# Kernel optimization log

Hardware: AMD Instinct MI355X
Metric: run time of the kernel (lower is better)

Reference implementation:

```python
import jax, jax.numpy as jnp
import numpy as np

H, K, V, F = 8, 64, 192, 192  # heads, key_size, value_size, num_position_features


def central_mask_features(distances, feature_size, seq_length):
    # distances: [L] float; returns [L, feature_size]
    pow_rate = np.exp(np.log(seq_length + 1) / feature_size).astype('float32')
    center_widths = jnp.power(pow_rate, jnp.arange(1, feature_size + 1, dtype=jnp.float32)) - 1.0
    return (center_widths[None, :] > jnp.abs(distances)[:, None]).astype(jnp.float32)


def positional_features(distances, feature_size, seq_length, symmetric=False):
    num_components = 1 if symmetric else 2
    emb = central_mask_features(distances, feature_size // num_components, seq_length)
    if not symmetric:
        emb = jnp.concatenate([emb, jnp.sign(distances)[:, None] * emb], axis=-1)
    return emb  # [L, feature_size]


def relative_shift(x):
    # x: [B, H, T1, T2] with T2 = 2*T1 - 1 -> [B, H, T1, T1]
    b, h, t1, t2 = x.shape
    x = jnp.pad(x, ((0, 0), (0, 0), (0, 0), (1, 0)))  # [B,H,T1,T2+1]
    x = x.reshape(b, h, t2 + 1, t1)[:, :, 1:, :]      # drop first row
    x = x.reshape(b, h, t1, t2)
    return x[..., : (t2 + 1) // 2]


def setup_inputs() -> dict:
    key = jax.random.key(0)
    ks = jax.random.split(key, 9)
    B, T, C = 2, 1536, 1536
    s = 1.0 / np.sqrt(C).astype('float32')
    return {
        'inputs': jax.random.normal(ks[0], (B, T, C), jnp.float32),
        'Wq': jax.random.normal(ks[1], (C, H * K), jnp.float32) * s,
        'Wk': jax.random.normal(ks[2], (C, H * K), jnp.float32) * s,
        'Wv': jax.random.normal(ks[3], (C, H * V), jnp.float32) * s,
        'Wrk': jax.random.normal(ks[4], (F, H * K), jnp.float32) * (1.0 / np.sqrt(F).astype('float32')),
        'We': jax.random.normal(ks[5], (H * V, H * V), jnp.float32) * (1.0 / np.sqrt(H * V).astype('float32')),
        'be': jnp.zeros((H * V,), jnp.float32),
        'r_w_bias': jax.random.normal(ks[6], (1, H, 1, K), jnp.float32) * 0.1,
        'r_r_bias': jax.random.normal(ks[7], (1, H, 1, K), jnp.float32) * 0.1,
    }


def reference(inputs, Wq, Wk, Wv, Wrk, We, be, r_w_bias, r_r_bias):
    B, T, C = inputs.shape

    def heads(x, d):  # [B,T,H*d] -> [B,H,T,d]
        return x.reshape(B, T, H, d).transpose(0, 2, 1, 3)

    q = heads(inputs @ Wq, K) * (K ** -0.5)
    k = heads(inputs @ Wk, K)
    v = heads(inputs @ Wv, V)

    # content logits: (q + r_w_bias) k^T -> [B,H,T,T]
    content_logits = jnp.einsum('bhqk,bhmk->bhqm', q + r_w_bias, k)

    # relative position logits
    distances = jnp.arange(-T + 1, T, dtype=jnp.float32)  # [2T-1]
    pe = positional_features(distances, F, T, symmetric=False)  # [2T-1, F]
    r_k = (pe @ Wrk).reshape(2 * T - 1, H, K).transpose(1, 0, 2)  # [H, 2T-1, K]
    rel_logits = jnp.einsum('bhqk,hmk->bhqm', q + r_r_bias, r_k)  # [B,H,T,2T-1]
    rel_logits = relative_shift(rel_logits)  # [B,H,T,T]

    logits = content_logits + rel_logits
    attn = jax.nn.softmax(logits, axis=-1)
    out = jnp.einsum('bhqm,bhmv->bhqv', attn, v)  # [B,H,T,V]
    out = out.transpose(0, 2, 1, 3).reshape(B, T, H * V)
    return out @ We + be
```

## Files before the change

kernel.cpp:

```cpp
#include <hip/hip_runtime.h>
#include <math.h>

#define HB 8
#define KD 64
#define VD 192
#define BT 2
#define TT 1536
#define CC 1536
#define HK (HB*KD)
#define HV (HB*VD)
#define QKVP 2560
#define LOG2E 1.44269504088896340736f

typedef float f32x4 __attribute__((ext_vector_type(4)));
typedef __bf16 bf16x8 __attribute__((ext_vector_type(8)));
typedef uint uint2v __attribute__((ext_vector_type(2)));

static __device__ __forceinline__ ushort f2bf(float f) {
  union { float f; uint u; } v; v.f = f;
  uint r = (v.u + 0x7FFFu + ((v.u >> 16) & 1u)) >> 16;
  return (ushort)r;
}
static __device__ __forceinline__ float bf2f(ushort u) {
  union { uint u; float f; } v; v.u = ((uint)u) << 16; return v.f;
}

static __device__ __forceinline__ f32x4 mfma_bf(bf16x8 a, bf16x8 b, f32x4 c) {
  return __builtin_amdgcn_mfma_f32_16x16x32_bf16(a, b, c, 0, 0, 0);
}

static __device__ __forceinline__ void gload_lds16(const ushort* g, ushort* l) {
  __builtin_amdgcn_global_load_lds(
      (const __attribute__((address_space(1))) unsigned int*)g,
      (__attribute__((address_space(3))) unsigned int*)l, 16, 0, 0);
}

__device__ __forceinline__ void storeC(float* p, float v) { *p = v; }
__device__ __forceinline__ void storeC(ushort* p, float v) { *p = f2bf(v); }

__global__ __launch_bounds__(256) void cast_bf16(
    const float* __restrict__ in, ushort* __restrict__ out, int n4)
{
  for (int i = blockIdx.x*blockDim.x + threadIdx.x; i < n4; i += gridDim.x*blockDim.x) {
    float4 v = ((const float4*)in)[i];
    ushort4 o; o.x = f2bf(v.x); o.y = f2bf(v.y); o.z = f2bf(v.z); o.w = f2bf(v.w);
    ((ushort4*)out)[i] = o;
  }
}

__global__ void tcast(const float* __restrict__ in, ushort* __restrict__ out, int R, int C, float scale)
{
  __shared__ float tile[32][33];
  const int bx = blockIdx.x * 32;
  const int by = blockIdx.y * 32;
  const int tx = threadIdx.x, ty = threadIdx.y;
  #pragma unroll
  for (int i = 0; i < 4; ++i)
    tile[ty + i*8][tx] = in[(size_t)(by + ty + i*8)*C + bx + tx];
  __syncthreads();
  #pragma unroll
  for (int i = 0; i < 4; ++i)
    out[(size_t)(bx + ty + i*8)*R + by + tx] = f2bf(tile[tx][ty + i*8] * scale);
}

__global__ void vtrans(const ushort* __restrict__ in, ushort* __restrict__ out)
{
  __shared__ ushort tile[32][33];
  const int bx = blockIdx.x * 32;
  const int by = blockIdx.y * 32;
  const int tx = threadIdx.x, ty = threadIdx.y;
  #pragma unroll
  for (int i = 0; i < 4; ++i)
    tile[ty + i*8][tx] = in[(size_t)(by + ty + i*8)*QKVP + 1024 + bx + tx];
  __syncthreads();
  #pragma unroll
  for (int i = 0; i < 4; ++i)
    out[(size_t)(bx + ty + i*8)*(BT*TT) + by + tx] = tile[tx][ty + i*8];
}

template<bool WITH_BIAS, typename OutT>
__global__ __launch_bounds__(256) void gemm_bf16(
    const ushort* __restrict__ A, const ushort* __restrict__ Bt,
    const float* __restrict__ bias, OutT* __restrict__ C,
    int M, int N, int Kd)
{
  __shared__ __align__(16) ushort As[128*64];
  __shared__ __align__(16) ushort Bs[128*64];
  const int t = threadIdx.x;
  const int w = t >> 6, lane = t & 63;
  const int lrow = lane & 15, lk8 = lane >> 4;
  const int row0 = blockIdx.y * 128, col0 = blockIdx.x * 128;
  const int wr = (w >> 1) * 64, wc = (w & 1) * 64;

  f32x4 acc[4][4];
  #pragma unroll
  for (int m = 0; m < 4; ++m)
    #pragma unroll
    for (int n = 0; n < 4; ++n) acc[m][n] = (f32x4){0.f,0.f,0.f,0.f};

  for (int k0 = 0; k0 < Kd; k0 += 64) {
    __syncthreads();
    #pragma unroll
    for (int j = 0; j < 4; ++j) {
      const int c = (w*4 + j)*64 + lane;
      const int r = c >> 3, cp = c & 7;
      const int sc = cp ^ (r & 7);
      gload_lds16(A  + (size_t)(row0 + r)*Kd + k0 + sc*8, As + c*8);
      gload_lds16(Bt + (size_t)(col0 + r)*Kd + k0 + sc*8, Bs + c*8);
    }
    __syncthreads();
    bf16x8 af[4][2], bfv[4][2];
    #pragma unroll
    for (int m = 0; m < 4; ++m) {
      const int r = wr + m*16 + lrow;
      #pragma unroll
      for (int kh = 0; kh < 2; ++kh) {
        const int k8 = lk8 + kh*4;
        af[m][kh] = *(const bf16x8*)&As[r*64 + ((k8 ^ (r & 7)) << 3)];
      }
    }
    #pragma unroll
    for (int n = 0; n < 4; ++n) {
      const int r = wc + n*16 + lrow;
      #pragma unroll
      for (int kh = 0; kh < 2; ++kh) {
        const int k8 = lk8 + kh*4;
        bfv[n][kh] = *(const bf16x8*)&Bs[r*64 + ((k8 ^ (r & 7)) << 3)];
      }
    }
    #pragma unroll
    for (int m = 0; m < 4; ++m)
      #pragma unroll
      for (int n = 0; n < 4; ++n) {
        acc[m][n] = mfma_bf(af[m][0], bfv[n][0], acc[m][n]);
        acc[m][n] = mfma_bf(af[m][1], bfv[n][1], acc[m][n]);
      }
  }
  #pragma unroll
  for (int m = 0; m < 4; ++m)
    #pragma unroll
    for (int n = 0; n < 4; ++n) {
      const int cg = col0 + wc + n*16 + lrow;
      const float bb = WITH_BIAS ? bias[cg] : 0.f;
      #pragma unroll
      for (int r = 0; r < 4; ++r) {
        const int rg = row0 + wr + m*16 + lk8*4 + r;
        storeC(&C[(size_t)rg*N + cg], acc[m][n][r] + bb);
      }
    }
}

__global__ __launch_bounds__(256) void wrk_suffix(
    const float* __restrict__ Wrk, float* __restrict__ S1, float* __restrict__ S2)
{
  const int c = blockIdx.x*blockDim.x + threadIdx.x;
  float a1 = 0.f, a2 = 0.f;
  S1[96*HK + c] = 0.f; S2[96*HK + c] = 0.f;
  for (int i = 95; i >= 0; --i) {
    a1 += Wrk[i*HK + c];
    a2 += Wrk[(96 + i)*HK + c];
    S1[i*HK + c] = a1; S2[i*HK + c] = a2;
  }
}

__global__ __launch_bounds__(256) void relk_fill(
    const float* __restrict__ S1, const float* __restrict__ S2,
    const float* __restrict__ rrb, ushort* __restrict__ rk, float* __restrict__ c2g)
{
  __shared__ float cw[96];
  __shared__ float red[512];
  __shared__ int i0s;
  const int t = threadIdx.x;
  const int m = blockIdx.x;
  if (t < 96) {
    double pr = exp(log((double)(TT + 1)) / 96.0);
    float prf = (float)pr;
    cw[t] = (float)pow((double)prf, (double)(t + 1)) - 1.0f;
  }
  __syncthreads();
  const int d = m - (TT - 1);
  const float ad = fabsf((float)d);
  if (t == 0) {
    int i0 = 96;
    for (int i = 0; i < 96; ++i) if (cw[i] > ad) { i0 = i; break; }
    i0s = i0;
  }
  __syncthreads();
  const float sg = (d > 0) ? 1.f : (d < 0 ? -1.f : 0.f);
  const int i0 = i0s;
  for (int c = t; c < HK; c += 256) {
    const float val = S1[i0*HK + c] + sg * S2[i0*HK + c];
    const ushort vb = f2bf(val);
    rk[(size_t)m * HK + c] = vb;
    red[c] = bf2f(vb) * rrb[c];
  }
  __syncthreads();
  if (t < 8) {
    float s = 0.f;
    #pragma unroll 16
    for (int i = 0; i < 64; ++i) s += red[t*64 + i];
    c2g[(size_t)t*(2*TT - 1) + m] = s * LOG2E;
  }
}

__global__ __launch_bounds__(256) void c1_kernel(
    const ushort* __restrict__ qkv, const float* __restrict__ rwb, float* __restrict__ c1g)
{
  const int idx = blockIdx.x*256 + threadIdx.x;
  const int h = idx & 7, row = idx >> 3;
  const ushort* kr = &qkv[(size_t)row*QKVP + 512 + h*KD];
  float s = 0.f;
  #pragma unroll 16
  for (int c = 0; c < 64; ++c) s += bf2f(kr[c]) * rwb[h*KD + c];
  c1g[h*(BT*TT) + row] = s * LOG2E;
}

__global__ __launch_bounds__(256) void attn_mfma(
    const ushort* __restrict__ qkv, const ushort* __restrict__ vTg,
    const ushort* __restrict__ rk,
    const float* __restrict__ c1g, const float* __restrict__ c2g,
    ushort* __restrict__ aout)
{
  __shared__ __align__(16) ushort ktL[32*64];
  __shared__ __align__(16) ushort rkbL[64*64];
  __shared__ __align__(16) ushort vTl[192*64];
  __shared__ __align__(16) ushort Pl[32][40];
  __shared__ __align__(16) float S1[32][34];
  __shared__ __align__(16) float S2[32][66];
  __shared__ float corrl[32], linv[32];

  const int t = threadIdx.x;
  const int wv = t >> 6, lane = t & 63;
  const int lrow = lane & 15, lk8 = lane >> 4;
  const int bid = blockIdx.x;
  const int qt = bid % (TT/32);
  const int h  = (bid / (TT/32)) % HB;
  const int b  = bid / ((TT/32) * HB);
  const int q0 = qt * 32;

  bf16x8 af[2][2];
  #pragma unroll
  for (int rt = 0; rt < 2; ++rt)
    #pragma unroll
    for (int kh = 0; kh < 2; ++kh)
      af[rt][kh] = *(const bf16x8*)&qkv[((size_t)(b*TT) + q0 + rt*16 + lrow)*QKVP + h*KD + kh*32 + lk8*8];

  if (t < 32) ((uint*)rkbL)[63*32 + t] = 0;

  const int kc_r = t >> 3, kc_p = t & 7;
  const ushort* ksrc = qkv + (size_t)(b*TT + kc_r)*QKVP + 512 + h*KD + (kc_p ^ (kc_r & 7))*8;
  ushort* kdst = ktL + t*8;
  const int rr0 = t >> 3, rp0 = t & 7;
  const int rr1 = (256 + t) >> 3, rp1 = t & 7;
  const ushort* rsrc0 = rk + (size_t)(TT - 32 - q0 + rr0)*HK + h*KD + (rp0 ^ (rr0 & 7))*8;
  const ushort* rsrc1 = rk + (size_t)(TT - 32 - q0 + rr1)*HK + h*KD + (rp1 ^ (rr1 & 7))*8;
  ushort* rdst0 = rkbL + t*8;
  ushort* rdst1 = rkbL + (256 + t)*8;
  const bool rval = t < 248;
  const ushort* vsrc[6]; ushort* vdst[6];
  #pragma unroll
  for (int W = 0; W < 6; ++W) {
    const int c = W*256 + t;
    const int vd = c >> 3, cpk = c & 7;
    vsrc[W] = vTg + (size_t)(h*VD + vd)*(BT*TT) + b*TT + (cpk ^ (vd & 7))*8;
    vdst[W] = vTl + c*8;
  }

  const int jk  = (wv & 1)*16 + lrow;
  const int j2a = (wv & 1)*32 + lrow;
  const int j2b = j2a + 16;
  const int rt_ = wv >> 1;

  f32x4 acc[2][3];
  #pragma unroll
  for (int i = 0; i < 2; ++i)
    #pragma unroll
    for (int j = 0; j < 3; ++j) acc[i][j] = (f32x4){0.f, 0.f, 0.f, 0.f};
  float m_i = -1e30f, l_i = 0.f;
  const int r_s = t >> 3;
  const int vsl = t & 7;

  gload_lds16(ksrc, kdst);               ksrc += 32*QKVP;
  gload_lds16(rsrc0, rdst0);             rsrc0 += 32*HK;
  if (rval) gload_lds16(rsrc1, rdst1);
  rsrc1 += 32*HK;

  for (int it = 0; it < 48; ++it) {
    const int kt0 = it << 5;
    const int mbase = kt0 - q0 + (TT - 32);
    const float c1v  = c1g[h*(BT*TT) + b*TT + kt0 + jk];
    const float c2v0 = c2g[(size_t)h*(2*TT - 1) + mbase + j2a];
    const float c2r  = c2g[(size_t)h*(2*TT - 1) + mbase + (j2b < 63 ? j2b : 62)];
    const float c2v1 = (j2b < 63) ? c2r : 0.f;

    if ((it & 1) == 0) {
      asm volatile("s_waitcnt lgkmcnt(0)" ::: "memory");
      __builtin_amdgcn_s_barrier();
      #pragma unroll
      for (int W = 0; W < 6; ++W) { gload_lds16(vsrc[W], vdst[W]); vsrc[W] += 64; }
      asm volatile("s_waitcnt vmcnt(6)" ::: "memory");
      __builtin_amdgcn_s_barrier();
    } else {
      asm volatile("s_waitcnt vmcnt(3)" ::: "memory");
      __builtin_amdgcn_s_barrier();
    }

    {
      bf16x8 b0 = *(const bf16x8*)&ktL[jk*64 + ((lk8 ^ (jk & 7)) << 3)];
      bf16x8 b1 = *(const bf16x8*)&ktL[jk*64 + (((lk8 + 4) ^ (jk & 7)) << 3)];
      f32x4 c0 = (f32x4){0.f, 0.f, 0.f, 0.f};
      c0 = mfma_bf(af[rt_][0], b0, c0);
      c0 = mfma_bf(af[rt_][1], b1, c0);
      #pragma unroll
      for (int r = 0; r < 4; ++r) S1[rt_*16 + lk8*4 + r][jk] = c0[r] + c1v;

      bf16x8 d0 = *(const bf16x8*)&rkbL[j2a*64 + ((lk8 ^ (j2a & 7)) << 3)];
      bf16x8 d1 = *(const bf16x8*)&rkbL[j2a*64 + (((lk8 + 4) ^ (j2a & 7)) << 3)];
      f32x4 ca = (f32x4){0.f, 0.f, 0.f, 0.f};
      ca = mfma_bf(af[rt_][0], d0, ca);
      ca = mfma_bf(af[rt_][1], d1, ca);
      #pragma unroll
      for (int r = 0; r < 4; ++r) S2[rt_*16 + lk8*4 + r][j2a] = ca[r] + c2v0;

      bf16x8 e0 = *(const bf16x8*)&rkbL[j2b*64 + ((lk8 ^ (j2b & 7)) << 3)];
      bf16x8 e1 = *(const bf16x8*)&rkbL[j2b*64 + (((lk8 + 4) ^ (j2b & 7)) << 3)];
      f32x4 cb = (f32x4){0.f, 0.f, 0.f, 0.f};
      cb = mfma_bf(af[rt_][0], e0, cb);
      cb = mfma_bf(af[rt_][1], e1, cb);
      #pragma unroll
      for (int r = 0; r < 4; ++r) S2[rt_*16 + lk8*4 + r][j2b] = cb[r] + c2v1;
    }
    asm volatile("s_waitcnt lgkmcnt(0)" ::: "memory");
    __builtin_amdgcn_s_barrier();
    if (it < 47) {
      gload_lds16(ksrc, kdst);               ksrc += 32*QKVP;
      gload_lds16(rsrc0, rdst0);             rsrc0 += 32*HK;
      if (rval) gload_lds16(rsrc1, rdst1);
      rsrc1 += 32*HK;
    }
    {
      float sv[4];
      #pragma unroll
      for (int i = 0; i < 4; ++i) {
        const int j = vsl*4 + i;
        sv[i] = S1[r_s][j] + S2[r_s][j - r_s + 31];
      }
      float lmax = fmaxf(fmaxf(sv[0], sv[1]), fmaxf(sv[2], sv[3]));
      #pragma unroll
      for (int s = 1; s < 8; s <<= 1) lmax = fmaxf(lmax, __shfl_xor(lmax, s, 64));
      const bool defer = (lmax <= m_i + 8.0f);
      const float m_new = defer ? m_i : fmaxf(m_i, lmax);
      const float corr  = defer ? 1.0f : exp2f(m_i - m_new);
      const float p0 = exp2f(sv[0] - m_new), p1 = exp2f(sv[1] - m_new);
      const float p2 = exp2f(sv[2] - m_new), p3 = exp2f(sv[3] - m_new);
      uint2v pw;
      pw.x = (uint)f2bf(p0) | ((uint)f2bf(p1) << 16);
      pw.y = (uint)f2bf(p2) | ((uint)f2bf(p3) << 16);
      *(uint2v*)&Pl[r_s][vsl*4] = pw;
      float lsum = (p0 + p1) + (p2 + p3);
      #pragma unroll
      for (int s = 1; s < 8; s <<= 1) lsum += __shfl_xor(lsum, s, 64);
      l_i = l_i * corr + lsum;
      m_i = m_new;
      if (vsl == 0) corrl[r_s] = corr;
    }
    if ((it & 1) == 0) { asm volatile("s_waitcnt vmcnt(3)" ::: "memory"); }
    asm volatile("s_waitcnt lgkmcnt(0)" ::: "memory");
    __builtin_amdgcn_s_barrier();
    {
      const int kh4 = (it & 1) * 4;
      float cr[2][4];
      #pragma unroll
      for (int rt = 0; rt < 2; ++rt)
        #pragma unroll
        for (int r = 0; r < 4; ++r) cr[rt][r] = corrl[rt*16 + lk8*4 + r];
      bool need = false;
      #pragma unroll
      for (int rt = 0; rt < 2; ++rt)
        #pragma unroll
        for (int r = 0; r < 4; ++r) need |= (cr[rt][r] != 1.0f);
      if (__any(need ? 1 : 0)) {
        #pragma unroll
        for (int rt = 0; rt < 2; ++rt)
          #pragma unroll
          for (int cc = 0; cc < 3; ++cc)
            #pragma unroll
            for (int r = 0; r < 4; ++r) acc[rt][cc][r] *= cr[rt][r];
      }
      #pragma unroll
      for (int rt = 0; rt < 2; ++rt) {
        const bf16x8 pa = *(const bf16x8*)&Pl[rt*16 + lrow][lk8*8];
        #pragma unroll
        for (int cc = 0; cc < 3; ++cc) {
          const int rv = (3*wv + cc)*16 + lrow;
          const bf16x8 bv = *(const bf16x8*)&vTl[rv*64 + (((kh4 + lk8) ^ (rv & 7)) << 3)];
          acc[rt][cc] = mfma_bf(pa, bv, acc[rt][cc]);
        }
      }
    }
  }
  if (vsl == 0) linv[r_s] = 1.0f / l_i;
  __syncthreads();
  #pragma unroll
  for (int rt = 0; rt < 2; ++rt) {
    #pragma unroll
    for (int cc = 0; cc < 3; ++cc) {
      const int colg = (3*wv + cc)*16 + lrow;
      #pragma unroll
      for (int r = 0; r < 4; ++r) {
        const int rowg = rt*16 + lk8*4 + r;
        aout[((size_t)(b*TT) + q0 + rowg) * HV + h*VD + colg] = f2bf(acc[rt][cc][r] * linv[rowg]);
      }
    }
  }
}

extern "C" void kernel_launch(void* const* d_in, const int* in_sizes, int n_in,
                              void* d_out, int out_size, void* d_ws, size_t ws_size,
                              hipStream_t stream)
{
  const float* X   = (const float*)d_in[0];
  const float* Wq  = (const float*)d_in[1];
  const float* Wk  = (const float*)d_in[2];
  const float* Wv  = (const float*)d_in[3];
  const float* Wrk = (const float*)d_in[4];
  const float* We  = (const float*)d_in[5];
  const float* be  = (const float*)d_in[6];
  const float* rwb = (const float*)d_in[7];
  const float* rrb = (const float*)d_in[8];
  float* out = (float*)d_out;

  char* ws = (char*)d_ws;
  ushort* Xb    = (ushort*)ws;                       ws += (size_t)3072*1536*2;
  ushort* Wqkvt = (ushort*)ws;                       ws += (size_t)2560*1536*2;
  ushort* Wet   = (ushort*)ws;                       ws += (size_t)1536*1536*2;
  float*  S1b   = (float*)ws;                        ws += (size_t)97*512*4;
  float*  S2b   = (float*)ws;                        ws += (size_t)97*512*4;
  ushort* qkvb  = (ushort*)ws;                       ws += (size_t)3072*2560*2;
  ushort* vTgb  = (ushort*)ws;                       ws += (size_t)1536*3072*2;
  ushort* rkb   = (ushort*)ws;                       ws += (size_t)3071*512*2;
  float*  c1g   = (float*)ws;                        ws += (size_t)8*3072*4;
  float*  c2g   = (float*)ws;                        ws += (size_t)8*3071*4;
  ushort* ao    = (ushort*)ws;

  dim3 blk(256);
  cast_bf16<<<2048, blk, 0, stream>>>(X, Xb, (3072*1536)/4);
  tcast<<<dim3(512/32, 1536/32),  dim3(32,8), 0, stream>>>(Wq, Wqkvt,                      1536, 512,  0.125f*LOG2E);
  tcast<<<dim3(512/32, 1536/32),  dim3(32,8), 0, stream>>>(Wk, Wqkvt + (size_t)512*1536,   1536, 512,  1.0f);
  tcast<<<dim3(1536/32, 1536/32), dim3(32,8), 0, stream>>>(Wv, Wqkvt + (size_t)1024*1536,  1536, 1536, 1.0f);
  tcast<<<dim3(1536/32, 1536/32), dim3(32,8), 0, stream>>>(We, Wet, 1536, 1536, 1.0f);
  wrk_suffix<<<2, blk, 0, stream>>>(Wrk, S1b, S2b);
  relk_fill<<<dim3(2*TT - 1), blk, 0, stream>>>(S1b, S2b, rrb, rkb, c2g);
  gemm_bf16<false, ushort><<<dim3(20, 24), blk, 0, stream>>>(Xb, Wqkvt, nullptr, qkvb, 3072, QKVP, 1536);
  vtrans<<<dim3(1536/32, 3072/32), dim3(32,8), 0, stream>>>(qkvb, vTgb);
  c1_kernel<<<96, blk, 0, stream>>>(qkvb, rwb, c1g);
  attn_mfma<<<dim3(BT*HB*(TT/32)), blk, 0, stream>>>(qkvb, vTgb, rkb, c1g, c2g, ao);
  gemm_bf16<true, float><<<dim3(12, 24), blk, 0, stream>>>(ao, Wet, be, out, 3072, 1536, 1536);
}
```

Measured before the change: 224.1 us.

## Widen attention key tile to 64 and restructure pipeline per iteration

The attention kernel now processes 64 keys per iteration instead of 32, halving loop trips and the associated barriers and online-softmax rescale steps. Each wave computes two S1 tiles and three S2 tiles, and each thread handles eight softmax columns with a 128-bit P store. V loads are issued after the P and V fragments are read into registers, and the c1/c2 bias values for the next tile are prefetched. Shared memory use grows considerably and launch_bounds requests 2 blocks per SM, which may limit occupancy or raise register pressure.

Measured after the change: 217.9 us. 1.03x faster.

```diff
diff --git a/kernel.cpp b/kernel.cpp
--- a/kernel.cpp
+++ b/kernel.cpp
@@ -14,7 +14,6 @@
 
 typedef float f32x4 __attribute__((ext_vector_type(4)));
 typedef __bf16 bf16x8 __attribute__((ext_vector_type(8)));
-typedef uint uint2v __attribute__((ext_vector_type(2)));
 
 static __device__ __forceinline__ ushort f2bf(float f) {
   union { float f; uint u; } v; v.f = f;
@@ -215,18 +214,18 @@
   c1g[h*(BT*TT) + row] = s * LOG2E;
 }
 
-__global__ __launch_bounds__(256) void attn_mfma(
+__global__ __launch_bounds__(256, 2) void attn_mfma(
     const ushort* __restrict__ qkv, const ushort* __restrict__ vTg,
     const ushort* __restrict__ rk,
     const float* __restrict__ c1g, const float* __restrict__ c2g,
     ushort* __restrict__ aout)
 {
-  __shared__ __align__(16) ushort ktL[32*64];
-  __shared__ __align__(16) ushort rkbL[64*64];
+  __shared__ __align__(16) ushort ktL[64*64];
+  __shared__ __align__(16) ushort rkbL[96*64];
   __shared__ __align__(16) ushort vTl[192*64];
-  __shared__ __align__(16) ushort Pl[32][40];
-  __shared__ __align__(16) float S1[32][34];
-  __shared__ __align__(16) float S2[32][66];
+  __shared__ __align__(16) ushort Pl[32][72];
+  __shared__ __align__(16) float S1[32][68];
+  __shared__ __align__(16) float S2[32][98];
   __shared__ float corrl[32], linv[32];
 
   const int t = threadIdx.x;
@@ -238,24 +237,33 @@
   const int b  = bid / ((TT/32) * HB);
   const int q0 = qt * 32;
 
-  bf16x8 af[2][2];
-  #pragma unroll
-  for (int rt = 0; rt < 2; ++rt)
-    #pragma unroll
-    for (int kh = 0; kh < 2; ++kh)
-      af[rt][kh] = *(const bf16x8*)&qkv[((size_t)(b*TT) + q0 + rt*16 + lrow)*QKVP + h*KD + kh*32 + lk8*8];
-
-  if (t < 32) ((uint*)rkbL)[63*32 + t] = 0;
-
-  const int kc_r = t >> 3, kc_p = t & 7;
-  const ushort* ksrc = qkv + (size_t)(b*TT + kc_r)*QKVP + 512 + h*KD + (kc_p ^ (kc_r & 7))*8;
-  ushort* kdst = ktL + t*8;
-  const int rr0 = t >> 3, rp0 = t & 7;
-  const int rr1 = (256 + t) >> 3, rp1 = t & 7;
-  const ushort* rsrc0 = rk + (size_t)(TT - 32 - q0 + rr0)*HK + h*KD + (rp0 ^ (rr0 & 7))*8;
-  const ushort* rsrc1 = rk + (size_t)(TT - 32 - q0 + rr1)*HK + h*KD + (rp1 ^ (rr1 & 7))*8;
-  ushort* rdst0 = rkbL + t*8;
-  ushort* rdst1 = rkbL + (256 + t)*8;
+  bf16x8 af00, af01, af10, af11;
+  {
+    const ushort* qbase = &qkv[((size_t)(b*TT) + q0 + lrow)*QKVP + h*KD];
+    af00 = *(const bf16x8*)&qbase[lk8*8];
+    af01 = *(const bf16x8*)&qbase[32 + lk8*8];
+    af10 = *(const bf16x8*)&qbase[16*QKVP + lk8*8];
+    af11 = *(const bf16x8*)&qbase[16*QKVP + 32 + lk8*8];
+  }
+
+  if (t < 32) ((uint*)rkbL)[95*32 + t] = 0;
+
+  const ushort* ksrc[2]; ushort* kdst[2];
+  #pragma unroll
+  for (int W = 0; W < 2; ++W) {
+    const int c = W*256 + t;
+    const int r = c >> 3, cp = c & 7;
+    ksrc[W] = qkv + (size_t)(b*TT + r)*QKVP + 512 + h*KD + (cp ^ (r & 7))*8;
+    kdst[W] = ktL + c*8;
+  }
+  const ushort* rsrc[3]; ushort* rdst[3];
+  #pragma unroll
+  for (int W = 0; W < 3; ++W) {
+    const int c = W*256 + t;
+    const int r = c >> 3, cp = c & 7;
+    rsrc[W] = rk + (size_t)(1504 - q0 + r)*HK + h*KD + (cp ^ (r & 7))*8;
+    rdst[W] = rkbL + c*8;
+  }
   const bool rval = t < 248;
   const ushort* vsrc[6]; ushort* vdst[6];
   #pragma unroll
@@ -266,10 +274,17 @@
     vdst[W] = vTl + c*8;
   }
 
-  const int jk  = (wv & 1)*16 + lrow;
-  const int j2a = (wv & 1)*32 + lrow;
-  const int j2b = j2a + 16;
-  const int rt_ = wv >> 1;
+  int jk_[2], rt1_[2], j2_[3], rt2_[3];
+  #pragma unroll
+  for (int s = 0; s < 2; ++s) {
+    const int idx = wv*2 + s;
+    rt1_[s] = idx >> 2; jk_[s] = (idx & 3)*16 + lrow;
+  }
+  #pragma unroll
+  for (int s = 0; s < 3; ++s) {
+    const int idx = wv*3 + s;
+    rt2_[s] = (idx >= 6) ? 1 : 0; j2_[s] = (idx - 6*rt2_[s])*16 + lrow;
+  }
 
   f32x4 acc[2][3];
   #pragma unroll
@@ -280,100 +295,135 @@
   const int r_s = t >> 3;
   const int vsl = t & 7;
 
-  gload_lds16(ksrc, kdst);               ksrc += 32*QKVP;
-  gload_lds16(rsrc0, rdst0);             rsrc0 += 32*HK;
-  if (rval) gload_lds16(rsrc1, rdst1);
-  rsrc1 += 32*HK;
-
-  for (int it = 0; it < 48; ++it) {
-    const int kt0 = it << 5;
-    const int mbase = kt0 - q0 + (TT - 32);
-    const float c1v  = c1g[h*(BT*TT) + b*TT + kt0 + jk];
-    const float c2v0 = c2g[(size_t)h*(2*TT - 1) + mbase + j2a];
-    const float c2r  = c2g[(size_t)h*(2*TT - 1) + mbase + (j2b < 63 ? j2b : 62)];
-    const float c2v1 = (j2b < 63) ? c2r : 0.f;
-
-    if ((it & 1) == 0) {
-      asm volatile("s_waitcnt lgkmcnt(0)" ::: "memory");
-      __builtin_amdgcn_s_barrier();
-      #pragma unroll
-      for (int W = 0; W < 6; ++W) { gload_lds16(vsrc[W], vdst[W]); vsrc[W] += 64; }
-      asm volatile("s_waitcnt vmcnt(6)" ::: "memory");
-      __builtin_amdgcn_s_barrier();
-    } else {
-      asm volatile("s_waitcnt vmcnt(3)" ::: "memory");
-      __builtin_amdgcn_s_barrier();
-    }
-
-    {
+  float c1p[2], c2p[3];
+  {
+    const int mb0 = -q0 + 1504;
+    #pragma unroll
+    for (int s = 0; s < 2; ++s) c1p[s] = c1g[h*(BT*TT) + b*TT + jk_[s]];
+    #pragma unroll
+    for (int s = 0; s < 3; ++s) {
+      const float v = c2g[(size_t)h*(2*TT - 1) + mb0 + (j2_[s] < 95 ? j2_[s] : 94)];
+      c2p[s] = (j2_[s] < 95) ? v : 0.f;
+    }
+  }
+  #pragma unroll
+  for (int W = 0; W < 2; ++W) { gload_lds16(ksrc[W], kdst[W]); ksrc[W] += 64*QKVP; }
+  gload_lds16(rsrc[0], rdst[0]);           rsrc[0] += 64*HK;
+  gload_lds16(rsrc[1], rdst[1]);           rsrc[1] += 64*HK;
+  if (rval) gload_lds16(rsrc[2], rdst[2]);
+  rsrc[2] += 64*HK;
+  #pragma unroll
+  for (int W = 0; W < 6; ++W) { gload_lds16(vsrc[W], vdst[W]); vsrc[W] += 64; }
+
+  for (int it = 0; it < 24; ++it) {
+    asm volatile("s_waitcnt vmcnt(6)" ::: "memory");
+    __builtin_amdgcn_s_barrier();
+    #pragma unroll
+    for (int s = 0; s < 2; ++s) {
+      const int rt = rt1_[s], jk = jk_[s];
+      const bf16x8 a0 = rt ? af10 : af00;
+      const bf16x8 a1 = rt ? af11 : af01;
       bf16x8 b0 = *(const bf16x8*)&ktL[jk*64 + ((lk8 ^ (jk & 7)) << 3)];
       bf16x8 b1 = *(const bf16x8*)&ktL[jk*64 + (((lk8 + 4) ^ (jk & 7)) << 3)];
       f32x4 c0 = (f32x4){0.f, 0.f, 0.f, 0.f};
-      c0 = mfma_bf(af[rt_][0], b0, c0);
-      c0 = mfma_bf(af[rt_][1], b1, c0);
-      #pragma unroll
-      for (int r = 0; r < 4; ++r) S1[rt_*16 + lk8*4 + r][jk] = c0[r] + c1v;
-
-      bf16x8 d0 = *(const bf16x8*)&rkbL[j2a*64 + ((lk8 ^ (j2a & 7)) << 3)];
-      bf16x8 d1 = *(const bf16x8*)&rkbL[j2a*64 + (((lk8 + 4) ^ (j2a & 7)) << 3)];
-      f32x4 ca = (f32x4){0.f, 0.f, 0.f, 0.f};
-      ca = mfma_bf(af[rt_][0], d0, ca);
-      ca = mfma_bf(af[rt_][1], d1, ca);
-      #pragma unroll
-      for (int r = 0; r < 4; ++r) S2[rt_*16 + lk8*4 + r][j2a] = ca[r] + c2v0;
-
-      bf16x8 e0 = *(const bf16x8*)&rkbL[j2b*64 + ((lk8 ^ (j2b & 7)) << 3)];
-      bf16x8 e1 = *(const bf16x8*)&rkbL[j2b*64 + (((lk8 + 4) ^ (j2b & 7)) << 3)];
-      f32x4 cb = (f32x4){0.f, 0.f, 0.f, 0.f};
-      cb = mfma_bf(af[rt_][0], e0, cb);
-      cb = mfma_bf(af[rt_][1], e1, cb);
-      #pragma unroll
-      for (int r = 0; r < 4; ++r) S2[rt_*16 + lk8*4 + r][j2b] = cb[r] + c2v1;
+      c0 = mfma_bf(a0, b0, c0);
+      c0 = mfma_bf(a1, b1, c0);
+      #pragma unroll
+      for (int r = 0; r < 4; ++r) S1[rt*16 + lk8*4 + r][jk] = c0[r] + c1p[s];
+    }
+    #pragma unroll
+    for (int s = 0; s < 3; ++s) {
+      const int rt = rt2_[s], j2 = j2_[s];
+      const bf16x8 a0 = rt ? af10 : af00;
+      const bf16x8 a1 = rt ? af11 : af01;
+      bf16x8 b0 = *(const bf16x8*)&rkbL[j2*64 + ((lk8 ^ (j2 & 7)) << 3)];
+      bf16x8 b1 = *(const bf16x8*)&rkbL[j2*64 + (((lk8 + 4) ^ (j2 & 7)) << 3)];
+      f32x4 c0 = (f32x4){0.f, 0.f, 0.f, 0.f};
+      c0 = mfma_bf(a0, b0, c0);
+      c0 = mfma_bf(a1, b1, c0);
+      #pragma unroll
+      for (int r = 0; r < 4; ++r) S2[rt*16 + lk8*4 + r][j2] = c0[r] + c2p[s];
     }
     asm volatile("s_waitcnt lgkmcnt(0)" ::: "memory");
     __builtin_amdgcn_s_barrier();
-    if (it < 47) {
-      gload_lds16(ksrc, kdst);               ksrc += 32*QKVP;
-      gload_lds16(rsrc0, rdst0);             rsrc0 += 32*HK;
-      if (rval) gload_lds16(rsrc1, rdst1);
-      rsrc1 += 32*HK;
+
+    if (it < 23) {
+      #pragma unroll
+      for (int W = 0; W < 2; ++W) { gload_lds16(ksrc[W], kdst[W]); ksrc[W] += 64*QKVP; }
+      gload_lds16(rsrc[0], rdst[0]);           rsrc[0] += 64*HK;
+      gload_lds16(rsrc[1], rdst[1]);           rsrc[1] += 64*HK;
+      if (rval) gload_lds16(rsrc[2], rdst[2]);
+      rsrc[2] += 64*HK;
+      const int kt0n = (it + 1) << 6;
+      const int mbn = kt0n - q0 + 1504;
+      #pragma unroll
+      for (int s = 0; s < 2; ++s) c1p[s] = c1g[h*(BT*TT) + b*TT + kt0n + jk_[s]];
+      #pragma unroll
+      for (int s = 0; s < 3; ++s) {
+        const float v = c2g[(size_t)h*(2*TT - 1) + mbn + (j2_[s] < 95 ? j2_[s] : 94)];
+        c2p[s] = (j2_[s] < 95) ? v : 0.f;
+      }
     }
     {
-      float sv[4];
-      #pragma unroll
-      for (int i = 0; i < 4; ++i) {
-        const int j = vsl*4 + i;
+      float sv[8];
+      #pragma unroll
+      for (int i = 0; i < 8; ++i) {
+        const int j = vsl*8 + i;
         sv[i] = S1[r_s][j] + S2[r_s][j - r_s + 31];
       }
-      float lmax = fmaxf(fmaxf(sv[0], sv[1]), fmaxf(sv[2], sv[3]));
+      float lmax = sv[0];
+      #pragma unroll
+      for (int i = 1; i < 8; ++i) lmax = fmaxf(lmax, sv[i]);
       #pragma unroll
       for (int s = 1; s < 8; s <<= 1) lmax = fmaxf(lmax, __shfl_xor(lmax, s, 64));
       const bool defer = (lmax <= m_i + 8.0f);
       const float m_new = defer ? m_i : fmaxf(m_i, lmax);
       const float corr  = defer ? 1.0f : exp2f(m_i - m_new);
-      const float p0 = exp2f(sv[0] - m_new), p1 = exp2f(sv[1] - m_new);
-      const float p2 = exp2f(sv[2] - m_new), p3 = exp2f(sv[3] - m_new);
-      uint2v pw;
-      pw.x = (uint)f2bf(p0) | ((uint)f2bf(p1) << 16);
-      pw.y = (uint)f2bf(p2) | ((uint)f2bf(p3) << 16);
-      *(uint2v*)&Pl[r_s][vsl*4] = pw;
-      float lsum = (p0 + p1) + (p2 + p3);
+      float p[8];
+      float lsum = 0.f;
+      #pragma unroll
+      for (int i = 0; i < 8; ++i) { p[i] = exp2f(sv[i] - m_new); lsum += p[i]; }
+      uint4 pw;
+      pw.x = (uint)f2bf(p[0]) | ((uint)f2bf(p[1]) << 16);
+      pw.y = (uint)f2bf(p[2]) | ((uint)f2bf(p[3]) << 16);
+      pw.z = (uint)f2bf(p[4]) | ((uint)f2bf(p[5]) << 16);
+      pw.w = (uint)f2bf(p[6]) | ((uint)f2bf(p[7]) << 16);
+      *(uint4*)&Pl[r_s][vsl*8] = pw;
       #pragma unroll
       for (int s = 1; s < 8; s <<= 1) lsum += __shfl_xor(lsum, s, 64);
       l_i = l_i * corr + lsum;
       m_i = m_new;
       if (vsl == 0) corrl[r_s] = corr;
     }
-    if ((it & 1) == 0) { asm volatile("s_waitcnt vmcnt(3)" ::: "memory"); }
+    if (it < 23) { asm volatile("s_waitcnt vmcnt(10)" ::: "memory"); }
+    else         { asm volatile("s_waitcnt vmcnt(0)"  ::: "memory"); }
     asm volatile("s_waitcnt lgkmcnt(0)" ::: "memory");
     __builtin_amdgcn_s_barrier();
+
     {
-      const int kh4 = (it & 1) * 4;
+      bf16x8 pa[2][2], bv[3][2];
+      #pragma unroll
+      for (int rt = 0; rt < 2; ++rt) {
+        pa[rt][0] = *(const bf16x8*)&Pl[rt*16 + lrow][lk8*8];
+        pa[rt][1] = *(const bf16x8*)&Pl[rt*16 + lrow][32 + lk8*8];
+      }
+      #pragma unroll
+      for (int cc = 0; cc < 3; ++cc) {
+        const int rv = (3*wv + cc)*16 + lrow;
+        bv[cc][0] = *(const bf16x8*)&vTl[rv*64 + ((lk8 ^ (rv & 7)) << 3)];
+        bv[cc][1] = *(const bf16x8*)&vTl[rv*64 + (((lk8 + 4) ^ (rv & 7)) << 3)];
+      }
       float cr[2][4];
       #pragma unroll
       for (int rt = 0; rt < 2; ++rt)
         #pragma unroll
         for (int r = 0; r < 4; ++r) cr[rt][r] = corrl[rt*16 + lk8*4 + r];
+      asm volatile("s_waitcnt lgkmcnt(0)" ::: "memory");
+      __builtin_amdgcn_s_barrier();
+      if (it < 23) {
+        #pragma unroll
+        for (int W = 0; W < 6; ++W) { gload_lds16(vsrc[W], vdst[W]); vsrc[W] += 64; }
+      }
       bool need = false;
       #pragma unroll
       for (int rt = 0; rt < 2; ++rt)
@@ -388,15 +438,12 @@
             for (int r = 0; r < 4; ++r) acc[rt][cc][r] *= cr[rt][r];
       }
       #pragma unroll
-      for (int rt = 0; rt < 2; ++rt) {
-        const bf16x8 pa = *(const bf16x8*)&Pl[rt*16 + lrow][lk8*8];
+      for (int rt = 0; rt < 2; ++rt)
         #pragma unroll
         for (int cc = 0; cc < 3; ++cc) {
-          const int rv = (3*wv + cc)*16 + lrow;
-          const bf16x8 bv = *(const bf16x8*)&vTl[rv*64 + (((kh4 + lk8) ^ (rv & 7)) << 3)];
-          acc[rt][cc] = mfma_bf(pa, bv, acc[rt][cc]);
+          acc[rt][cc] = mfma_bf(pa[rt][0], bv[cc][0], acc[rt][cc]);
+          acc[rt][cc] = mfma_bf(pa[rt][1], bv[cc][1], acc[rt][cc]);
         }
-      }
     }
   }
   if (vsl == 0) linv[r_s] = 1.0f / l_i;
```

## Compute softmax in MFMA operand layout and pipeline V tiles per 32-key step

Applied to the files above, without the earlier changes.

The attention kernel now has each wave compute the softmax probabilities directly in the MFMA A-operand register layout, so the P and correction-factor shared-memory buffers go away. Row statistics and correction factors are exchanged with cross-lane shuffles instead. V is now staged in 32-key tiles double-buffered against compute, with the c1/c2 bias values prefetched one iteration ahead. Shared memory shrinks and launch bounds request 3 blocks per CU to raise occupancy. In exchange every wave redundantly computes softmax for all 32 rows, the accumulator rescale always runs, and the synchronisation is more intricate.

Measured after the change: 256.5 us. +14.4%, slower.

```diff
diff --git a/kernel.cpp b/kernel.cpp
--- a/kernel.cpp
+++ b/kernel.cpp
@@ -14,7 +14,6 @@
 
 typedef float f32x4 __attribute__((ext_vector_type(4)));
 typedef __bf16 bf16x8 __attribute__((ext_vector_type(8)));
-typedef uint uint2v __attribute__((ext_vector_type(2)));
 
 static __device__ __forceinline__ ushort f2bf(float f) {
   union { float f; uint u; } v; v.f = f;
@@ -215,7 +214,7 @@
   c1g[h*(BT*TT) + row] = s * LOG2E;
 }
 
-__global__ __launch_bounds__(256) void attn_mfma(
+__global__ __launch_bounds__(256, 3) void attn_mfma(
     const ushort* __restrict__ qkv, const ushort* __restrict__ vTg,
     const ushort* __restrict__ rk,
     const float* __restrict__ c1g, const float* __restrict__ c2g,
@@ -223,11 +222,9 @@
 {
   __shared__ __align__(16) ushort ktL[32*64];
   __shared__ __align__(16) ushort rkbL[64*64];
-  __shared__ __align__(16) ushort vTl[192*64];
-  __shared__ __align__(16) ushort Pl[32][40];
-  __shared__ __align__(16) float S1[32][34];
-  __shared__ __align__(16) float S2[32][66];
-  __shared__ float corrl[32], linv[32];
+  __shared__ __align__(16) ushort vTl[192*32];
+  __shared__ __align__(16) float S1[32][36];
+  __shared__ __align__(16) float S2[32][68];
 
   const int t = threadIdx.x;
   const int wv = t >> 6, lane = t & 63;
@@ -238,31 +235,31 @@
   const int b  = bid / ((TT/32) * HB);
   const int q0 = qt * 32;
 
-  bf16x8 af[2][2];
-  #pragma unroll
-  for (int rt = 0; rt < 2; ++rt)
-    #pragma unroll
-    for (int kh = 0; kh < 2; ++kh)
-      af[rt][kh] = *(const bf16x8*)&qkv[((size_t)(b*TT) + q0 + rt*16 + lrow)*QKVP + h*KD + kh*32 + lk8*8];
-
+  bf16x8 af00, af01, af10, af11;
+  {
+    const ushort* qbase = &qkv[((size_t)(b*TT) + q0 + lrow)*QKVP + h*KD];
+    af00 = *(const bf16x8*)&qbase[lk8*8];
+    af01 = *(const bf16x8*)&qbase[32 + lk8*8];
+    af10 = *(const bf16x8*)&qbase[16*QKVP + lk8*8];
+    af11 = *(const bf16x8*)&qbase[16*QKVP + 32 + lk8*8];
+  }
   if (t < 32) ((uint*)rkbL)[63*32 + t] = 0;
 
   const int kc_r = t >> 3, kc_p = t & 7;
   const ushort* ksrc = qkv + (size_t)(b*TT + kc_r)*QKVP + 512 + h*KD + (kc_p ^ (kc_r & 7))*8;
   ushort* kdst = ktL + t*8;
-  const int rr0 = t >> 3, rp0 = t & 7;
-  const int rr1 = (256 + t) >> 3, rp1 = t & 7;
-  const ushort* rsrc0 = rk + (size_t)(TT - 32 - q0 + rr0)*HK + h*KD + (rp0 ^ (rr0 & 7))*8;
-  const ushort* rsrc1 = rk + (size_t)(TT - 32 - q0 + rr1)*HK + h*KD + (rp1 ^ (rr1 & 7))*8;
+  const int rr0 = t >> 3, rr1 = (256 + t) >> 3, rpc = t & 7;
+  const ushort* rsrc0 = rk + (size_t)(1504 - q0 + rr0)*HK + h*KD + (rpc ^ (rr0 & 7))*8;
+  const ushort* rsrc1 = rk + (size_t)(1504 - q0 + rr1)*HK + h*KD + (rpc ^ (rr1 & 7))*8;
   ushort* rdst0 = rkbL + t*8;
   ushort* rdst1 = rkbL + (256 + t)*8;
   const bool rval = t < 248;
-  const ushort* vsrc[6]; ushort* vdst[6];
-  #pragma unroll
-  for (int W = 0; W < 6; ++W) {
+  const ushort* vsrc[3]; ushort* vdst[3];
+  #pragma unroll
+  for (int W = 0; W < 3; ++W) {
     const int c = W*256 + t;
-    const int vd = c >> 3, cpk = c & 7;
-    vsrc[W] = vTg + (size_t)(h*VD + vd)*(BT*TT) + b*TT + (cpk ^ (vd & 7))*8;
+    const int vd = c >> 2, cpk = c & 3;
+    vsrc[W] = vTg + (size_t)(h*VD + vd)*(BT*TT) + b*TT + ((cpk ^ (vd & 3)))*8;
     vdst[W] = vTl + c*8;
   }
 
@@ -276,57 +273,51 @@
   for (int i = 0; i < 2; ++i)
     #pragma unroll
     for (int j = 0; j < 3; ++j) acc[i][j] = (f32x4){0.f, 0.f, 0.f, 0.f};
-  float m_i = -1e30f, l_i = 0.f;
-  const int r_s = t >> 3;
-  const int vsl = t & 7;
-
+  float m_i[2] = {-1e30f, -1e30f};
+  float l_i[2] = {0.f, 0.f};
+
+  float c1v, c2v0, c2v1;
   gload_lds16(ksrc, kdst);               ksrc += 32*QKVP;
   gload_lds16(rsrc0, rdst0);             rsrc0 += 32*HK;
   if (rval) gload_lds16(rsrc1, rdst1);
   rsrc1 += 32*HK;
+  {
+    const int mb = -q0 + 1504;
+    c1v  = c1g[h*(BT*TT) + b*TT + jk];
+    c2v0 = c2g[(size_t)h*(2*TT - 1) + mb + j2a];
+    const float cr = c2g[(size_t)h*(2*TT - 1) + mb + (j2b < 63 ? j2b : 62)];
+    c2v1 = (j2b < 63) ? cr : 0.f;
+  }
+  #pragma unroll
+  for (int W = 0; W < 3; ++W) { gload_lds16(vsrc[W], vdst[W]); vsrc[W] += 32; }
 
   for (int it = 0; it < 48; ++it) {
-    const int kt0 = it << 5;
-    const int mbase = kt0 - q0 + (TT - 32);
-    const float c1v  = c1g[h*(BT*TT) + b*TT + kt0 + jk];
-    const float c2v0 = c2g[(size_t)h*(2*TT - 1) + mbase + j2a];
-    const float c2r  = c2g[(size_t)h*(2*TT - 1) + mbase + (j2b < 63 ? j2b : 62)];
-    const float c2v1 = (j2b < 63) ? c2r : 0.f;
-
-    if ((it & 1) == 0) {
-      asm volatile("s_waitcnt lgkmcnt(0)" ::: "memory");
-      __builtin_amdgcn_s_barrier();
-      #pragma unroll
-      for (int W = 0; W < 6; ++W) { gload_lds16(vsrc[W], vdst[W]); vsrc[W] += 64; }
-      asm volatile("s_waitcnt vmcnt(6)" ::: "memory");
-      __builtin_amdgcn_s_barrier();
-    } else {
-      asm volatile("s_waitcnt vmcnt(3)" ::: "memory");
-      __builtin_amdgcn_s_barrier();
-    }
-
+    asm volatile("s_waitcnt vmcnt(6)" ::: "memory");
+    __builtin_amdgcn_s_barrier();
     {
+      const bf16x8 a0 = rt_ ? af10 : af00;
+      const bf16x8 a1 = rt_ ? af11 : af01;
       bf16x8 b0 = *(const bf16x8*)&ktL[jk*64 + ((lk8 ^ (jk & 7)) << 3)];
       bf16x8 b1 = *(const bf16x8*)&ktL[jk*64 + (((lk8 + 4) ^ (jk & 7)) << 3)];
       f32x4 c0 = (f32x4){0.f, 0.f, 0.f, 0.f};
-      c0 = mfma_bf(af[rt_][0], b0, c0);
-      c0 = mfma_bf(af[rt_][1], b1, c0);
+      c0 = mfma_bf(a0, b0, c0);
+      c0 = mfma_bf(a1, b1, c0);
       #pragma unroll
       for (int r = 0; r < 4; ++r) S1[rt_*16 + lk8*4 + r][jk] = c0[r] + c1v;
 
       bf16x8 d0 = *(const bf16x8*)&rkbL[j2a*64 + ((lk8 ^ (j2a & 7)) << 3)];
       bf16x8 d1 = *(const bf16x8*)&rkbL[j2a*64 + (((lk8 + 4) ^ (j2a & 7)) << 3)];
       f32x4 ca = (f32x4){0.f, 0.f, 0.f, 0.f};
-      ca = mfma_bf(af[rt_][0], d0, ca);
-      ca = mfma_bf(af[rt_][1], d1, ca);
+      ca = mfma_bf(a0, d0, ca);
+      ca = mfma_bf(a1, d1, ca);
       #pragma unroll
       for (int r = 0; r < 4; ++r) S2[rt_*16 + lk8*4 + r][j2a] = ca[r] + c2v0;
 
       bf16x8 e0 = *(const bf16x8*)&rkbL[j2b*64 + ((lk8 ^ (j2b & 7)) << 3)];
       bf16x8 e1 = *(const bf16x8*)&rkbL[j2b*64 + (((lk8 + 4) ^ (j2b & 7)) << 3)];
       f32x4 cb = (f32x4){0.f, 0.f, 0.f, 0.f};
-      cb = mfma_bf(af[rt_][0], e0, cb);
-      cb = mfma_bf(af[rt_][1], e1, cb);
+      cb = mfma_bf(a0, e0, cb);
+      cb = mfma_bf(a1, e1, cb);
       #pragma unroll
       for (int r = 0; r < 4; ++r) S2[rt_*16 + lk8*4 + r][j2b] = cb[r] + c2v1;
     }
@@ -337,79 +328,88 @@
       gload_lds16(rsrc0, rdst0);             rsrc0 += 32*HK;
       if (rval) gload_lds16(rsrc1, rdst1);
       rsrc1 += 32*HK;
-    }
-    {
-      float sv[4];
-      #pragma unroll
-      for (int i = 0; i < 4; ++i) {
-        const int j = vsl*4 + i;
-        sv[i] = S1[r_s][j] + S2[r_s][j - r_s + 31];
-      }
-      float lmax = fmaxf(fmaxf(sv[0], sv[1]), fmaxf(sv[2], sv[3]));
-      #pragma unroll
-      for (int s = 1; s < 8; s <<= 1) lmax = fmaxf(lmax, __shfl_xor(lmax, s, 64));
-      const bool defer = (lmax <= m_i + 8.0f);
-      const float m_new = defer ? m_i : fmaxf(m_i, lmax);
-      const float corr  = defer ? 1.0f : exp2f(m_i - m_new);
-      const float p0 = exp2f(sv[0] - m_new), p1 = exp2f(sv[1] - m_new);
-      const float p2 = exp2f(sv[2] - m_new), p3 = exp2f(sv[3] - m_new);
-      uint2v pw;
-      pw.x = (uint)f2bf(p0) | ((uint)f2bf(p1) << 16);
-      pw.y = (uint)f2bf(p2) | ((uint)f2bf(p3) << 16);
-      *(uint2v*)&Pl[r_s][vsl*4] = pw;
-      float lsum = (p0 + p1) + (p2 + p3);
-      #pragma unroll
-      for (int s = 1; s < 8; s <<= 1) lsum += __shfl_xor(lsum, s, 64);
-      l_i = l_i * corr + lsum;
-      m_i = m_new;
-      if (vsl == 0) corrl[r_s] = corr;
-    }
-    if ((it & 1) == 0) { asm volatile("s_waitcnt vmcnt(3)" ::: "memory"); }
+      const int kt0n = (it + 1) << 5;
+      const int mbn = kt0n - q0 + 1504;
+      c1v  = c1g[h*(BT*TT) + b*TT + kt0n + jk];
+      c2v0 = c2g[(size_t)h*(2*TT - 1) + mbn + j2a];
+      const float cr = c2g[(size_t)h*(2*TT - 1) + mbn + (j2b < 63 ? j2b : 62)];
+      c2v1 = (j2b < 63) ? cr : 0.f;
+    }
+    bf16x8 pa[2];
+    float corr[2];
+    #pragma unroll
+    for (int rt = 0; rt < 2; ++rt) {
+      const int row = rt*16 + lrow;
+      const float4 a0 = *(const float4*)&S1[row][lk8*8];
+      const float4 a1 = *(const float4*)&S1[row][lk8*8 + 4];
+      const int off = lk8*8 - row + 31;
+      float sv[8];
+      sv[0] = a0.x + S2[row][off + 0]; sv[1] = a0.y + S2[row][off + 1];
+      sv[2] = a0.z + S2[row][off + 2]; sv[3] = a0.w + S2[row][off + 3];
+      sv[4] = a1.x + S2[row][off + 4]; sv[5] = a1.y + S2[row][off + 5];
+      sv[6] = a1.z + S2[row][off + 6]; sv[7] = a1.w + S2[row][off + 7];
+      float lm = fmaxf(fmaxf(fmaxf(sv[0], sv[1]), fmaxf(sv[2], sv[3])),
+                       fmaxf(fmaxf(sv[4], sv[5]), fmaxf(sv[6], sv[7])));
+      lm = fmaxf(lm, __shfl_xor(lm, 16, 64));
+      lm = fmaxf(lm, __shfl_xor(lm, 32, 64));
+      const bool defer = (lm <= m_i[rt] + 8.0f);
+      const float m_new = defer ? m_i[rt] : fmaxf(m_i[rt], lm);
+      corr[rt] = defer ? 1.0f : exp2f(m_i[rt] - m_new);
+      float p[8], ls = 0.f;
+      #pragma unroll
+      for (int i = 0; i < 8; ++i) { p[i] = exp2f(sv[i] - m_new); ls += p[i]; }
+      ls += __shfl_xor(ls, 16, 64);
+      ls += __shfl_xor(ls, 32, 64);
+      l_i[rt] = l_i[rt] * corr[rt] + ls;
+      m_i[rt] = m_new;
+      union { uint4 u; bf16x8 v; } pk;
+      pk.u.x = (uint)f2bf(p[0]) | ((uint)f2bf(p[1]) << 16);
+      pk.u.y = (uint)f2bf(p[2]) | ((uint)f2bf(p[3]) << 16);
+      pk.u.z = (uint)f2bf(p[4]) | ((uint)f2bf(p[5]) << 16);
+      pk.u.w = (uint)f2bf(p[6]) | ((uint)f2bf(p[7]) << 16);
+      pa[rt] = pk.v;
+    }
+    float cracc[2][4];
+    #pragma unroll
+    for (int rt = 0; rt < 2; ++rt)
+      #pragma unroll
+      for (int r = 0; r < 4; ++r) cracc[rt][r] = __shfl(corr[rt], lk8*4 + r, 64);
+    if (it < 47) { asm volatile("s_waitcnt vmcnt(6)" ::: "memory"); }
+    else         { asm volatile("s_waitcnt vmcnt(0)" ::: "memory"); }
+    __builtin_amdgcn_s_barrier();
+    bf16x8 bv[3];
+    #pragma unroll
+    for (int cc = 0; cc < 3; ++cc) {
+      const int rv = (3*wv + cc)*16 + lrow;
+      bv[cc] = *(const bf16x8*)&vTl[rv*32 + ((lk8 ^ (rv & 3)) << 3)];
+    }
     asm volatile("s_waitcnt lgkmcnt(0)" ::: "memory");
     __builtin_amdgcn_s_barrier();
-    {
-      const int kh4 = (it & 1) * 4;
-      float cr[2][4];
-      #pragma unroll
-      for (int rt = 0; rt < 2; ++rt)
+    if (it < 47) {
+      #pragma unroll
+      for (int W = 0; W < 3; ++W) { gload_lds16(vsrc[W], vdst[W]); vsrc[W] += 32; }
+    }
+    #pragma unroll
+    for (int rt = 0; rt < 2; ++rt)
+      #pragma unroll
+      for (int cc = 0; cc < 3; ++cc) {
+        f32x4 a = acc[rt][cc];
         #pragma unroll
-        for (int r = 0; r < 4; ++r) cr[rt][r] = corrl[rt*16 + lk8*4 + r];
-      bool need = false;
-      #pragma unroll
-      for (int rt = 0; rt < 2; ++rt)
-        #pragma unroll
-        for (int r = 0; r < 4; ++r) need |= (cr[rt][r] != 1.0f);
-      if (__any(need ? 1 : 0)) {
-        #pragma unroll
-        for (int rt = 0; rt < 2; ++rt)
-          #pragma unroll
-          for (int cc = 0; cc < 3; ++cc)
-            #pragma unroll
-            for (int r = 0; r < 4; ++r) acc[rt][cc][r] *= cr[rt][r];
-      }
-      #pragma unroll
-      for (int rt = 0; rt < 2; ++rt) {
-        const bf16x8 pa = *(const bf16x8*)&Pl[rt*16 + lrow][lk8*8];
-        #pragma unroll
-        for (int cc = 0; cc < 3; ++cc) {
-          const int rv = (3*wv + cc)*16 + lrow;
-          const bf16x8 bv = *(const bf16x8*)&vTl[rv*64 + (((kh4 + lk8) ^ (rv & 7)) << 3)];
-          acc[rt][cc] = mfma_bf(pa, bv, acc[rt][cc]);
-        }
-      }
-    }
-  }
-  if (vsl == 0) linv[r_s] = 1.0f / l_i;
-  __syncthreads();
+        for (int r = 0; r < 4; ++r) a[r] *= cracc[rt][r];
+        acc[rt][cc] = mfma_bf(pa[rt], bv[cc], a);
+      }
+  }
+  const float li0 = 1.0f / l_i[0], li1 = 1.0f / l_i[1];
   #pragma unroll
   for (int rt = 0; rt < 2; ++rt) {
     #pragma unroll
-    for (int cc = 0; cc < 3; ++cc) {
-      const int colg = (3*wv + cc)*16 + lrow;
-      #pragma unroll
-      for (int r = 0; r < 4; ++r) {
-        const int rowg = rt*16 + lk8*4 + r;
-        aout[((size_t)(b*TT) + q0 + rowg) * HV + h*VD + colg] = f2bf(acc[rt][cc][r] * linv[rowg]);
+    for (int r = 0; r < 4; ++r) {
+      const float inv = __shfl(rt ? li1 : li0, lk8*4 + r, 64);
+      const int rowg = rt*16 + lk8*4 + r;
+      #pragma unroll
+      for (int cc = 0; cc < 3; ++cc) {
+        const int colg = (3*wv + cc)*16 + lrow;
+        aout[((size_t)(b*TT) + q0 + rowg) * HV + h*VD + colg] = f2bf(acc[rt][cc][r] * inv);
       }
     }
   }
```
